# Optimization experiments

Measured on AMD Instinct MI355X. Metric: run time of the kernel, lower is better.

The kernel has to match this reference:

```python
import jax, jax.numpy as jnp
import numpy as np

K = 20          # top-k neighbors each side
C_THRESH = 0.0  # nnPU clipping threshold
GAMMA = 1.0
PRIOR_PRIME = 0.5


def _l2_normalize(x, eps=1e-12):
    # matches torch F.normalize(dim=1): x / max(||x||, eps)
    n = jnp.maximum(jnp.linalg.norm(x, axis=1, keepdims=True), eps)
    return x / n


def setup_inputs() -> dict:
    key = jax.random.key(0)
    k1, k2 = jax.random.split(key)
    N, C = 4096, 256
    return {
        "input": jax.random.normal(k1, (N, C), dtype=jnp.float32),
        "target": jax.random.normal(k2, (N, C), dtype=jnp.float32),
    }


def reference(input, target):
    pred_norm = _l2_normalize(input)      # [N, C]
    target_norm = _l2_normalize(target)   # [N, C]
    n = input.shape[0]

    # cosine distance in [0, 1]
    dist = (1.0 - pred_norm @ target_norm.T) * 0.5  # [N, N]

    eye = jnp.eye(n, dtype=bool)
    dist_ap = jnp.diagonal(dist)  # mask[i] selects only the diagonal -> max is dist[i,i]

    # off-diagonal top-k smallest / largest per row (mask diagonal with +/-inf)
    d_for_min = jnp.where(eye, jnp.inf, dist)
    d_for_max = jnp.where(eye, -jnp.inf, dist)
    neg_down_k, _ = jax.lax.top_k(-d_for_min, K)  # k smallest -> negated
    down_k = -neg_down_k                          # [N, K]
    up_k, _ = jax.lax.top_k(d_for_max, K)         # [N, K]

    sum_pos_unl = down_k.sum(axis=-1) + up_k.sum(axis=-1)  # [N]

    n_positive = 1.0
    n_unlabeled = 2.0 * K
    positive_risk = (PRIOR_PRIME / n_positive) * dist_ap
    negative_risk = -((1.0 - PRIOR_PRIME) / (n_positive * n_unlabeled)) * sum_pos_unl

    loss_i = jnp.where(negative_risk < C_THRESH,
                       -GAMMA * negative_risk,
                       positive_risk + negative_risk)
    return loss_i.mean()
```

## Files before the change

### kernel.cpp

```cpp
#include <hip/hip_runtime.h>
#include <hip/hip_bf16.h>
#include <math.h>

#define NROW 4096
#define CDIM 256
#define KSEL 20

typedef __attribute__((ext_vector_type(8))) short short8_t;
typedef __attribute__((ext_vector_type(4))) float f32x4;
typedef const __attribute__((address_space(1))) unsigned g_u32;
typedef __attribute__((address_space(3))) unsigned l_u32;

__device__ __forceinline__ unsigned sad_u8(unsigned a, unsigned b, unsigned c) {
    unsigned d;
    asm("v_sad_u8 %0, %1, %2, %3" : "=v"(d) : "v"(a), "v"(b), "v"(c));
    return d;
}

__global__ __launch_bounds__(256) void prep_kernel(const float* __restrict__ A,
                                                   const float* __restrict__ B,
                                                   ushort* __restrict__ An,
                                                   ushort* __restrict__ Bn) {
    const int bid = blockIdx.x;
    const int row = bid & (NROW - 1);
    const float* __restrict__ X = (bid < NROW) ? A : B;
    ushort* __restrict__ Y = (bid < NROW) ? An : Bn;
    const int tid = threadIdx.x;
    float v = X[(size_t)row * CDIM + tid];
    float s = v * v;
#pragma unroll
    for (int off = 32; off; off >>= 1) s += __shfl_xor(s, off, 64);
    __shared__ float p[4];
    __shared__ float rsh;
    if ((tid & 63) == 0) p[tid >> 6] = s;
    __syncthreads();
    if (tid == 0) rsh = 1.0f / fmaxf(sqrtf(p[0] + p[1] + p[2] + p[3]), 1e-12f);
    __syncthreads();
    __hip_bfloat16 h = __float2bfloat16(v * rsh);
    Y[(size_t)row * CDIM + tid] = *(ushort*)&h;
}

__global__ __launch_bounds__(256) void gemm16_kernel(const ushort* __restrict__ An,
                                                     const ushort* __restrict__ Bn,
                                                     unsigned char* __restrict__ dist8,
                                                     int r0) {
    const int tid  = threadIdx.x;
    const int lane = tid & 63;
    const int wid  = tid >> 6;
    const int wm = wid >> 1, wn = wid & 1;
    const int ib = blockIdx.y * 128;
    const int i0 = r0 + ib;
    const int j0 = blockIdx.x * 128;
    const int lr  = lane & 15;
    const int lk8 = (lane >> 4) * 8;

    __shared__ ushort As[128 * 64];
    __shared__ ushort Bs[128 * 64];

    const int srow = tid >> 3;
    const int scol = (tid & 7) * 8;
    const unsigned wbase = (unsigned)(wid * 1024);

    f32x4 acc[4][4];
#pragma unroll
    for (int m = 0; m < 4; ++m)
#pragma unroll
        for (int n = 0; n < 4; ++n) acc[m][n] = (f32x4){0.f, 0.f, 0.f, 0.f};

#pragma unroll
    for (int ks = 0; ks < CDIM / 64; ++ks) {
        const int k0 = ks * 64;
#pragma unroll
        for (int r = 0; r < 4; ++r) {
            const ushort* ga = An + (size_t)(i0 + r * 32 + srow) * CDIM + k0 + scol;
            __builtin_amdgcn_global_load_lds((g_u32*)ga,
                (l_u32*)((char*)As + r * 4096 + wbase), 16, 0, 0);
        }
#pragma unroll
        for (int r = 0; r < 4; ++r) {
            const ushort* gb = Bn + (size_t)(j0 + r * 32 + srow) * CDIM + k0 + scol;
            __builtin_amdgcn_global_load_lds((g_u32*)gb,
                (l_u32*)((char*)Bs + r * 4096 + wbase), 16, 0, 0);
        }
        __syncthreads();

#pragma unroll
        for (int kk = 0; kk < 2; ++kk) {
            const int coff = kk * 32 + lk8;
            short8_t a[4], b[4];
#pragma unroll
            for (int m = 0; m < 4; ++m)
                a[m] = *(const short8_t*)&As[(wm * 64 + m * 16 + lr) * 64 + coff];
#pragma unroll
            for (int n = 0; n < 4; ++n)
                b[n] = *(const short8_t*)&Bs[(wn * 64 + n * 16 + lr) * 64 + coff];
#pragma unroll
            for (int m = 0; m < 4; ++m)
#pragma unroll
                for (int n = 0; n < 4; ++n)
                    acc[m][n] = __builtin_amdgcn_mfma_f32_16x16x32_bf16(a[m], b[n], acc[m][n], 0, 0, 0);
        }
        __syncthreads();
    }

    const int orow = (lane >> 4) * 4;
    const int ocol = lane & 15;
#pragma unroll
    for (int m = 0; m < 4; ++m) {
#pragma unroll
        for (int q = 0; q < 4; ++q) {
            const int irow = ib + wm * 64 + m * 16 + orow + q;
#pragma unroll
            for (int n = 0; n < 4; ++n) {
                float d = (1.0f - acc[m][n][q]) * 0.5f;
                d = fminf(fmaxf(d, 0.0f), 1.0f);
                unsigned key = __float2uint_rn(d * 127.0f);
                dist8[(size_t)irow * NROW + (j0 + wn * 64 + n * 16 + ocol)] = (unsigned char)key;
            }
        }
    }
}

__global__ __launch_bounds__(256) void select_kernel(const unsigned char* __restrict__ dist8,
                                                     float* __restrict__ loss, int r0) {
    const int tid  = threadIdx.x;
    const int lane = tid & 63;
    const int wid  = tid >> 6;
    const int rb   = blockIdx.x * 4 + wid;
    const int grow = r0 + rb;

    const uint4* __restrict__ P = (const uint4*)(dist8 + (size_t)rb * NROW);
    unsigned w[16];
#pragma unroll
    for (int i = 0; i < 4; ++i) {
        uint4 v = P[i * 64 + lane];
        w[4 * i + 0] = v.x; w[4 * i + 1] = v.y;
        w[4 * i + 2] = v.z; w[4 * i + 3] = v.w;
    }
    const unsigned dku = (unsigned)dist8[(size_t)rb * NROW + grow];
    const unsigned M = 0x80808080u;
    const unsigned zero = 0u;

    unsigned rs = 0;
#pragma unroll
    for (int i = 0; i < 16; ++i) rs = sad_u8(w[i], zero, rs);

    int lo1 = 0, hi1 = 128, clo = 0;
    int lo2 = -1, hi2 = 127, chi = 0;
#pragma unroll 1
    for (int it = 0; it < 7; ++it) {
        const int mid1 = (lo1 + hi1) >> 1;
        const int mid2 = (lo2 + hi2) >> 1;
        const unsigned C1 = (unsigned)(127 + mid1) * 0x01010101u;
        const unsigned C2 = (unsigned)(128 + mid2) * 0x01010101u;
        unsigned a1 = 0, a2 = 0;
#pragma unroll
        for (int i = 0; i < 16; ++i) {
            a1 = sad_u8((C1 - w[i]) & M, zero, a1);
            a2 = sad_u8((C2 - w[i]) & M, zero, a2);
        }
        int cc = (int)((a1 >> 7) | ((a2 >> 7) << 16));
#pragma unroll
        for (int off = 32; off; off >>= 1) cc += __shfl_xor(cc, off, 64);
        cc = __builtin_amdgcn_readfirstlane(cc);
        const int c1 = (cc & 0xFFFF) - ((dku < (unsigned)mid1) ? 1 : 0);
        const int c2 = (4096 - (cc >> 16)) - (((int)dku > mid2) ? 1 : 0);
        if (c1 < KSEL) { lo1 = mid1; clo = c1; } else hi1 = mid1;
        if (c2 < KSEL) { hi2 = mid2; chi = c2; } else lo2 = mid2;
    }
    const int Tmin = lo1, Tmax = hi2;

    const unsigned CA = (unsigned)(127 + Tmin) * 0x01010101u;
    const unsigned CB = (unsigned)(128 + Tmax) * 0x01010101u;
    unsigned sA = 0, sB = 0;
#pragma unroll
    for (int i = 0; i < 16; ++i) {
        const unsigned mA = ((CA - w[i]) & M) >> 7;
        sA = sad_u8(w[i] & ((mA << 8) - mA), zero, sA);
        const unsigned mB = ((CB - w[i]) & M) >> 7;
        sB = sad_u8(w[i] & ((mB << 8) - mB), zero, sB);
    }
#pragma unroll
    for (int off = 32; off; off >>= 1) {
        rs += __shfl_xor(rs, off, 64);
        sA += __shfl_xor(sA, off, 64);
        sB += __shfl_xor(sB, off, 64);
    }

    const int sum_min_i = (int)sA - ((dku < (unsigned)Tmin) ? (int)dku : 0)
                        + (KSEL - clo) * Tmin;
    const int sum_gt    = (int)(rs - sB);
    const int sum_max_i = sum_gt - (((int)dku > Tmax) ? (int)dku : 0)
                        + (KSEL - chi) * Tmax;

    if (lane == 0) {
        const float inv = 1.0f / 127.0f;
        const float total = (float)(sum_min_i + sum_max_i) * inv;
        const float dap = (float)dku * inv;
        const float neg = -0.0125f * total;
        const float pos = 0.5f * dap;
        loss[grow] = (neg < 0.f) ? -neg : (pos + neg);
    }
}

__global__ __launch_bounds__(256) void finalize_kernel(const float* __restrict__ loss,
                                                       float* __restrict__ out) {
    const int tid = threadIdx.x;
    float s = 0.f;
    for (int k = tid; k < NROW; k += 256) s += loss[k];
#pragma unroll
    for (int off = 32; off; off >>= 1) s += __shfl_xor(s, off, 64);
    __shared__ float p[4];
    if ((tid & 63) == 0) p[tid >> 6] = s;
    __syncthreads();
    if (tid == 0) out[0] = (p[0] + p[1] + p[2] + p[3]) * (1.0f / (float)NROW);
}

extern "C" void kernel_launch(void* const* d_in, const int* in_sizes, int n_in,
                              void* d_out, int out_size, void* d_ws, size_t ws_size,
                              hipStream_t stream) {
    const float* A = (const float*)d_in[0];
    const float* B = (const float*)d_in[1];

    char* ws = (char*)d_ws;
    const size_t norm_bytes = (size_t)NROW * CDIM * 2;
    ushort* An    = (ushort*)ws;
    ushort* Bn    = (ushort*)(ws + norm_bytes);
    float*  lossv = (float*)(ws + 2 * norm_bytes);
    unsigned char* dist8 = (unsigned char*)(ws + 2 * norm_bytes + NROW * 4);
    const size_t fixed = 2 * norm_bytes + (size_t)NROW * 4;

    int band = NROW;
    while (band > 128 && fixed + (size_t)band * NROW > ws_size) band >>= 1;

    prep_kernel<<<2 * NROW, 256, 0, stream>>>(A, B, An, Bn);
    for (int r0 = 0; r0 < NROW; r0 += band) {
        gemm16_kernel<<<dim3(NROW / 128, band / 128), 256, 0, stream>>>(An, Bn, dist8, r0);
        select_kernel<<<band / 4, 256, 0, stream>>>(dist8, lossv, r0);
    }
    finalize_kernel<<<1, 256, 0, stream>>>(lossv, (float*)d_out);
}
```

Baseline: 48.74 us.

## Double-buffer GEMM LDS tiles, remap workgroups across XCDs, vectorize row normalization

The GEMM kernel now double-buffers its A/B LDS tiles so the global-to-LDS copy for the next K slice is issued before the MFMAs on the current slice. It also remaps flat workgroup IDs so consecutive blocks land on different chiplets in a strided pattern, aiming for better L2 reuse. The prep kernel now normalizes one row per wavefront using float4 loads and ushort4 stores, dropping the shared-memory reduction and two barriers. Risks: the doubled LDS use may lower occupancy, and the workgroup remap hardcodes 32 column tiles and assumes the block count is divisible by 8.

```diff
diff --git a/kernel.cpp b/kernel.cpp
--- a/kernel.cpp
+++ b/kernel.cpp
@@ -21,23 +21,26 @@
                                                    const float* __restrict__ B,
                                                    ushort* __restrict__ An,
                                                    ushort* __restrict__ Bn) {
-    const int bid = blockIdx.x;
-    const int row = bid & (NROW - 1);
-    const float* __restrict__ X = (bid < NROW) ? A : B;
-    ushort* __restrict__ Y = (bid < NROW) ? An : Bn;
-    const int tid = threadIdx.x;
-    float v = X[(size_t)row * CDIM + tid];
-    float s = v * v;
+    const int tid  = threadIdx.x;
+    const int lane = tid & 63;
+    const int wid  = tid >> 6;
+    const int r    = blockIdx.x * 4 + wid;
+    const int row  = r & (NROW - 1);
+    const float* __restrict__ X = (r < NROW) ? A : B;
+    ushort* __restrict__ Y = (r < NROW) ? An : Bn;
+
+    const float4 v = ((const float4*)(X + (size_t)row * CDIM))[lane];
+    float s = v.x * v.x + v.y * v.y + v.z * v.z + v.w * v.w;
 #pragma unroll
     for (int off = 32; off; off >>= 1) s += __shfl_xor(s, off, 64);
-    __shared__ float p[4];
-    __shared__ float rsh;
-    if ((tid & 63) == 0) p[tid >> 6] = s;
-    __syncthreads();
-    if (tid == 0) rsh = 1.0f / fmaxf(sqrtf(p[0] + p[1] + p[2] + p[3]), 1e-12f);
-    __syncthreads();
-    __hip_bfloat16 h = __float2bfloat16(v * rsh);
-    Y[(size_t)row * CDIM + tid] = *(ushort*)&h;
+    const float rinv = 1.0f / fmaxf(sqrtf(s), 1e-12f);
+
+    ushort4 o;
+    __hip_bfloat16 h0 = __float2bfloat16(v.x * rinv); o.x = *(ushort*)&h0;
+    __hip_bfloat16 h1 = __float2bfloat16(v.y * rinv); o.y = *(ushort*)&h1;
+    __hip_bfloat16 h2 = __float2bfloat16(v.z * rinv); o.z = *(ushort*)&h2;
+    __hip_bfloat16 h3 = __float2bfloat16(v.w * rinv); o.w = *(ushort*)&h3;
+    ((ushort4*)(Y + (size_t)row * CDIM))[lane] = o;
 }
 
 __global__ __launch_bounds__(256) void gemm16_kernel(const ushort* __restrict__ An,
@@ -48,14 +51,21 @@
     const int lane = tid & 63;
     const int wid  = tid >> 6;
     const int wm = wid >> 1, wn = wid & 1;
-    const int ib = blockIdx.y * 128;
+
+    const int nwg  = gridDim.x * gridDim.y;
+    const int flat = blockIdx.y * gridDim.x + blockIdx.x;
+    const int wg   = (flat & 7) * (nwg >> 3) + (flat >> 3);
+    const int bx   = wg & 31;
+    const int byt  = wg >> 5;
+
+    const int ib = byt * 128;
     const int i0 = r0 + ib;
-    const int j0 = blockIdx.x * 128;
+    const int j0 = bx * 128;
     const int lr  = lane & 15;
     const int lk8 = (lane >> 4) * 8;
 
-    __shared__ ushort As[128 * 64];
-    __shared__ ushort Bs[128 * 64];
+    __shared__ ushort As[2][128 * 64];
+    __shared__ ushort Bs[2][128 * 64];
 
     const int srow = tid >> 3;
     const int scol = (tid & 7) * 8;
@@ -68,32 +78,41 @@
         for (int n = 0; n < 4; ++n) acc[m][n] = (f32x4){0.f, 0.f, 0.f, 0.f};
 
 #pragma unroll
-    for (int ks = 0; ks < CDIM / 64; ++ks) {
-        const int k0 = ks * 64;
-#pragma unroll
-        for (int r = 0; r < 4; ++r) {
-            const ushort* ga = An + (size_t)(i0 + r * 32 + srow) * CDIM + k0 + scol;
-            __builtin_amdgcn_global_load_lds((g_u32*)ga,
-                (l_u32*)((char*)As + r * 4096 + wbase), 16, 0, 0);
-        }
-#pragma unroll
-        for (int r = 0; r < 4; ++r) {
-            const ushort* gb = Bn + (size_t)(j0 + r * 32 + srow) * CDIM + k0 + scol;
-            __builtin_amdgcn_global_load_lds((g_u32*)gb,
-                (l_u32*)((char*)Bs + r * 4096 + wbase), 16, 0, 0);
-        }
-        __syncthreads();
-
+    for (int r = 0; r < 4; ++r) {
+        const ushort* ga = An + (size_t)(i0 + r * 32 + srow) * CDIM + scol;
+        __builtin_amdgcn_global_load_lds((g_u32*)ga,
+            (l_u32*)((char*)As[0] + r * 4096 + wbase), 16, 0, 0);
+        const ushort* gb = Bn + (size_t)(j0 + r * 32 + srow) * CDIM + scol;
+        __builtin_amdgcn_global_load_lds((g_u32*)gb,
+            (l_u32*)((char*)Bs[0] + r * 4096 + wbase), 16, 0, 0);
+    }
+    __syncthreads();
+
+#pragma unroll
+    for (int ks = 0; ks < 4; ++ks) {
+        const int cur = ks & 1;
+        if (ks < 3) {
+            const int k0 = (ks + 1) * 64;
+#pragma unroll
+            for (int r = 0; r < 4; ++r) {
+                const ushort* ga = An + (size_t)(i0 + r * 32 + srow) * CDIM + k0 + scol;
+                __builtin_amdgcn_global_load_lds((g_u32*)ga,
+                    (l_u32*)((char*)As[cur ^ 1] + r * 4096 + wbase), 16, 0, 0);
+                const ushort* gb = Bn + (size_t)(j0 + r * 32 + srow) * CDIM + k0 + scol;
+                __builtin_amdgcn_global_load_lds((g_u32*)gb,
+                    (l_u32*)((char*)Bs[cur ^ 1] + r * 4096 + wbase), 16, 0, 0);
+            }
+        }
 #pragma unroll
         for (int kk = 0; kk < 2; ++kk) {
             const int coff = kk * 32 + lk8;
             short8_t a[4], b[4];
 #pragma unroll
             for (int m = 0; m < 4; ++m)
-                a[m] = *(const short8_t*)&As[(wm * 64 + m * 16 + lr) * 64 + coff];
+                a[m] = *(const short8_t*)&As[cur][(wm * 64 + m * 16 + lr) * 64 + coff];
 #pragma unroll
             for (int n = 0; n < 4; ++n)
-                b[n] = *(const short8_t*)&Bs[(wn * 64 + n * 16 + lr) * 64 + coff];
+                b[n] = *(const short8_t*)&Bs[cur][(wn * 64 + n * 16 + lr) * 64 + coff];
 #pragma unroll
             for (int m = 0; m < 4; ++m)
 #pragma unroll
@@ -233,7 +252,7 @@
     int band = NROW;
     while (band > 128 && fixed + (size_t)band * NROW > ws_size) band >>= 1;
 
-    prep_kernel<<<2 * NROW, 256, 0, stream>>>(A, B, An, Bn);
+    prep_kernel<<<2 * NROW / 4, 256, 0, stream>>>(A, B, An, Bn);
     for (int r0 = 0; r0 < NROW; r0 += band) {
         gemm16_kernel<<<dim3(NROW / 128, band / 128), 256, 0, stream>>>(An, Bn, dist8, r0);
         select_kernel<<<band / 4, 256, 0, stream>>>(dist8, lossv, r0);
```

Result: faster. 46.26 us (-5.1%).
